# Kernel tuning notes

Hardware: AMD Instinct MI355X
Metric: run time of the kernel (lower is better)

## Reference

```python
import jax, jax.numpy as jnp
import numpy as np

NUM_GRAPHS = 256


def _lin_params(key, fan_in, fan_out):
    k1, k2 = jax.random.split(key)
    bound = 1.0 / np.sqrt(fan_in)
    W = jax.random.uniform(k1, (fan_in, fan_out), jnp.float32, -bound, bound)
    b = jax.random.uniform(k2, (fan_out,), jnp.float32, -bound, bound)
    return W, b


def setup_inputs() -> dict:
    key = jax.random.key(0)
    ks = jax.random.split(key, 12)
    N, E, F = 100000, 3200000, 32
    x = jax.random.normal(ks[0], (N, F), jnp.float32)
    edge_index = jax.random.randint(ks[1], (2, E), 0, N, jnp.int64)
    batch = jnp.sort(jax.random.randint(ks[2], (N,), 0, NUM_GRAPHS, jnp.int64))
    W1, b1 = _lin_params(ks[3], 32, 32)   # conv1
    W2, b2 = _lin_params(ks[4], 32, 24)   # conv2
    Wg, bg = _lin_params(ks[5], 24, 32)   # g_fcn1
    Wt, bt = _lin_params(ks[6], 32, 2)    # t_fcn1
    Wn1, bn1 = _lin_params(ks[7], 24, 16)  # n_fcn1
    Wn2, bn2 = _lin_params(ks[8], 16, 1)   # n_fcn2
    Wb1, bb1 = _lin_params(ks[9], 24, 16)  # b_fcn1
    Wb2, bb2 = _lin_params(ks[10], 16, 3)  # b_fcn2
    return {"x": x, "edge_index": edge_index, "batch": batch,
            "W1": W1, "b1": b1, "W2": W2, "b2": b2,
            "Wg": Wg, "bg": bg, "Wt": Wt, "bt": bt,
            "Wn1": Wn1, "bn1": bn1, "Wn2": Wn2, "bn2": bn2,
            "Wb1": Wb1, "bb1": bb1, "Wb2": Wb2, "bb2": bb2}


def _gcn_conv(x, edge_index, W, b):
    """PyG GCNConv: self-loops + symmetric normalization + linear."""
    N = x.shape[0]
    h = x @ W  # [N, out]
    loop = jnp.arange(N, dtype=edge_index.dtype)
    row = jnp.concatenate([edge_index[0], loop])  # source
    col = jnp.concatenate([edge_index[1], loop])  # target
    deg = jax.ops.segment_sum(jnp.ones_like(col, dtype=h.dtype), col, num_segments=N)
    dinv = jnp.where(deg > 0, jax.lax.rsqrt(deg), 0.0)
    norm = dinv[row] * dinv[col]  # [E+N]
    out = jax.ops.segment_sum(h[row] * norm[:, None], col, num_segments=N)
    return out + b


def _segment_softmax(v, seg, num_seg):
    """Softmax over nodes within each graph (leading axis)."""
    m = jax.ops.segment_max(v, seg, num_segments=num_seg)
    e = jnp.exp(v - m[seg])
    s = jax.ops.segment_sum(e, seg, num_segments=num_seg)
    return e / s[seg]


def reference(x, edge_index, batch, W1, b1, W2, b2, Wg, bg, Wt, bt,
              Wn1, bn1, Wn2, bn2, Wb1, bb1, Wb2, bb2):
    h = jax.nn.relu(_gcn_conv(x, edge_index, W1, b1))          # [N,32]
    h = jax.nn.relu(_gcn_conv(h, edge_index, W2, b2))          # [N,24]
    # global mean pool
    cnt = jax.ops.segment_sum(jnp.ones((h.shape[0],), h.dtype), batch, num_segments=NUM_GRAPHS)
    g = jax.ops.segment_sum(h, batch, num_segments=NUM_GRAPHS) / jnp.maximum(cnt, 1.0)[:, None]
    g = g @ Wg + bg                                            # [G,32]
    t = jax.nn.softmax(g @ Wt + bt, axis=1)                    # [G,2]
    n = jax.nn.relu(h @ Wn1 + bn1) @ Wn2 + bn2                 # [N,1]
    n = _segment_softmax(n, batch, NUM_GRAPHS)                 # per-graph softmax over nodes
    b_feat = jax.ops.segment_sum(n * h, batch, num_segments=NUM_GRAPHS)  # global_add_pool of n*x
    bb = jax.nn.relu(b_feat @ Wb1 + bb1) @ Wb2 + bb2           # [G,3]
    bb = jax.nn.softmax(bb, axis=0)                            # dim=0 softmax as in source
    return (t, n, bb)
```

## Files before the change

### kernel.cpp

```cpp
#include <hip/hip_runtime.h>
#include <math.h>

#define NG 256
#define NBLK 256

#define S1F 16.0f
#define IS1F 0.0625f
#define S2F 64.0f
#define IS2F 0.015625f

typedef __attribute__((ext_vector_type(2))) float f32x2;

__device__ __forceinline__ unsigned enc4(float f0, float f1, float f2, float f3) {
    int r = __builtin_amdgcn_cvt_pk_fp8_f32(f0, f1, 0, false);
    r = __builtin_amdgcn_cvt_pk_fp8_f32(f2, f3, r, true);
    return (unsigned)r;
}
__device__ __forceinline__ void acc8p(uint2 v, f32x2 (&a)[4]) {
    a[0] += __builtin_amdgcn_cvt_pk_f32_fp8((int)v.x, false);
    a[1] += __builtin_amdgcn_cvt_pk_f32_fp8((int)v.x, true);
    a[2] += __builtin_amdgcn_cvt_pk_f32_fp8((int)v.y, false);
    a[3] += __builtin_amdgcn_cvt_pk_f32_fp8((int)v.y, true);
}

__global__ __launch_bounds__(256) void hist_bucket_kernel(
        const int* __restrict__ col, int* __restrict__ blockOff,
        int* __restrict__ bucketTot, int E, int NB) {
    __shared__ int h[512];
    h[threadIdx.x] = 0; h[threadIdx.x + 256] = 0;
    __syncthreads();
    const int chunk = (((E + NBLK - 1) / NBLK) + 3) & ~3;
    const int beg = blockIdx.x * chunk;
    const int end = min(beg + chunk, E);
    if ((E & 3) == 0) {
        int e = beg + threadIdx.x * 4;
        for (; e + 3 < end; e += 1024) {
            int4 c = *(const int4*)(col + e);
            atomicAdd(&h[c.x >> 8], 1);
            atomicAdd(&h[c.y >> 8], 1);
            atomicAdd(&h[c.z >> 8], 1);
            atomicAdd(&h[c.w >> 8], 1);
        }
        for (; e < end; e++) atomicAdd(&h[col[e] >> 8], 1);
    } else {
        for (int e = beg + threadIdx.x; e < end; e += 256)
            atomicAdd(&h[col[e] >> 8], 1);
    }
    __syncthreads();
    for (int t = threadIdx.x; t < NB; t += 256) {
        int off = atomicAdd(&bucketTot[t], h[t]);
        blockOff[t * NBLK + blockIdx.x] = off;
    }
}

__global__ __launch_bounds__(512) void tiny_scan_kernel(
        const int* __restrict__ bucketTot, int* __restrict__ bucketBase, int NB) {
    __shared__ int part[512];
    const int t = threadIdx.x;
    int v = (t < NB) ? bucketTot[t] : 0;
    part[t] = v;
    __syncthreads();
    for (int o = 1; o < 512; o <<= 1) {
        int u = (t >= o) ? part[t - o] : 0;
        __syncthreads();
        part[t] += u;
        __syncthreads();
    }
    if (t < NB) bucketBase[t] = part[t] - v;
    if (t == NB) bucketBase[NB] = part[NB - 1];
    if (t == 511 && NB == 512) bucketBase[NB] = part[511];
}

__global__ __launch_bounds__(256) void scatter_pairs_kernel(
        const int* __restrict__ ei, const int* __restrict__ blockOff,
        const int* __restrict__ bucketBase, int* __restrict__ pairs, int E, int NB) {
    __shared__ int cur[512];
    for (int t = threadIdx.x; t < NB; t += 256)
        cur[t] = bucketBase[t] + blockOff[t * NBLK + blockIdx.x];
    __syncthreads();
    const int chunk = (((E + NBLK - 1) / NBLK) + 3) & ~3;
    const int beg = blockIdx.x * chunk;
    const int end = min(beg + chunk, E);
    if ((E & 3) == 0) {
        int e = beg + threadIdx.x * 4;
        for (; e + 3 < end; e += 1024) {
            int4 s = *(const int4*)(ei + e);
            int4 tg = *(const int4*)(ei + E + e);
            int p0 = atomicAdd(&cur[tg.x >> 8], 1);
            pairs[p0] = (int)(((unsigned)(tg.x & 255) << 17) | (unsigned)s.x);
            int p1 = atomicAdd(&cur[tg.y >> 8], 1);
            pairs[p1] = (int)(((unsigned)(tg.y & 255) << 17) | (unsigned)s.y);
            int p2 = atomicAdd(&cur[tg.z >> 8], 1);
            pairs[p2] = (int)(((unsigned)(tg.z & 255) << 17) | (unsigned)s.z);
            int p3 = atomicAdd(&cur[tg.w >> 8], 1);
            pairs[p3] = (int)(((unsigned)(tg.w & 255) << 17) | (unsigned)s.w);
        }
        for (; e < end; e++) {
            int src = ei[e];
            int tgt = ei[E + e];
            int pos = atomicAdd(&cur[tgt >> 8], 1);
            pairs[pos] = (int)(((unsigned)(tgt & 255) << 17) | (unsigned)src);
        }
    } else {
        for (int e = beg + threadIdx.x; e < end; e += 256) {
            int src = ei[e];
            int tgt = ei[E + e];
            int pos = atomicAdd(&cur[tgt >> 8], 1);
            pairs[pos] = (int)(((unsigned)(tgt & 255) << 17) | (unsigned)src);
        }
    }
}

__global__ __launch_bounds__(256) void csr_bucket_kernel(
        const int* __restrict__ pairs, const int* __restrict__ bucketBase,
        int* __restrict__ rowptr, int* __restrict__ adj,
        float* __restrict__ dinv, int N, int E) {
    __shared__ int h[256];
    __shared__ int sc[256];
    __shared__ int cur[256];
    const int b = blockIdx.x, t = threadIdx.x;
    const int base = bucketBase[b];
    const int end = bucketBase[b + 1];
    h[t] = 0;
    __syncthreads();
    for (int i = base + t; i < end; i += 256)
        atomicAdd(&h[(unsigned)pairs[i] >> 17], 1);
    __syncthreads();
    const int v = h[t];
    sc[t] = v;
    __syncthreads();
    for (int o = 1; o < 256; o <<= 1) {
        int u = (t >= o) ? sc[t - o] : 0;
        __syncthreads();
        sc[t] += u;
        __syncthreads();
    }
    const int ex = sc[t] - v;
    const int node = (b << 8) + t;
    if (node < N) {
        rowptr[node] = base + ex;
        dinv[node] = rsqrtf((float)v + 1.0f);
    }
    cur[t] = base + ex;
    __syncthreads();
    for (int i = base + t; i < end; i += 256) {
        unsigned p = (unsigned)pairs[i];
        int pos = atomicAdd(&cur[p >> 17], 1);
        adj[pos] = (int)(p & 0x1FFFFu);
    }
    if (b == 0 && t == 0) rowptr[N] = E;
}

__global__ __launch_bounds__(256) void bounds_kernel(
        const int* __restrict__ batch, int* __restrict__ starts, int N) {
    int i = blockIdx.x * blockDim.x + threadIdx.x;
    if (i >= N) return;
    int b = batch[i];
    int bp = (i == 0) ? -1 : batch[i - 1];
    for (int g = bp + 1; g <= b; g++) starts[g] = i;
    if (i == N - 1)
        for (int g = b + 1; g <= NG; g++) starts[g] = N;
}

__global__ __launch_bounds__(256) void hs1_kernel(
        const float* __restrict__ x, const float* __restrict__ W,
        const float* __restrict__ dinv, unsigned* __restrict__ hs, int N) {
    __shared__ float Ws[32 * 32];
    __shared__ float tmp[8][32];
    for (int t = threadIdx.x; t < 1024; t += blockDim.x) Ws[t] = W[t];
    __syncthreads();
    const int tid = threadIdx.x;
    const int node = blockIdx.x * 8 + (tid >> 5);
    const int n = tid >> 5, f = tid & 31;
    if (node < N) {
        const float* xr = x + (size_t)node * 32;
        float acc = 0.f;
#pragma unroll
        for (int k = 0; k < 32; k++) acc += xr[k] * Ws[k * 32 + f];
        tmp[n][f] = acc * dinv[node] * S1F;
        if (f < 8)
            hs[(size_t)node * 8 + f] = enc4(tmp[n][4 * f], tmp[n][4 * f + 1],
                                            tmp[n][4 * f + 2], tmp[n][4 * f + 3]);
    }
}

__global__ __launch_bounds__(256) void gather1_kernel(
        const int* __restrict__ rowptr, const int* __restrict__ adj,
        const uint2* __restrict__ hs1q, const float* __restrict__ dinv,
        const float* __restrict__ b1, const float* __restrict__ W2,
        unsigned* __restrict__ hs2out, int N) {
    __shared__ float W2s[32 * 24];
    __shared__ float b1s[32];
    __shared__ float h1row[16][32];
    __shared__ float hs2t[16][32];
    const int tid = threadIdx.x;
    for (int t = tid; t < 768; t += 256) W2s[t] = W2[t];
    if (tid < 32) b1s[tid] = b1[tid];

    const int g = tid >> 5;
    const int l = tid & 31;
    const int f8 = l & 3;
    const int e8 = l >> 2;
    const int n0 = (blockIdx.x * 8 + g) * 2;
    const int n1 = n0 + 1;
    const bool val0 = n0 < N;
    const bool val1 = n1 < N;

    int beg0 = 0, cnt0 = 0, beg1 = 0, cnt1 = 0;
    if (val0) {
        int2 rp = *(const int2*)(rowptr + n0);
        beg0 = rp.x; cnt0 = rp.y - rp.x;
        if (val1) { int e2 = rowptr[n0 + 2]; beg1 = rp.y; cnt1 = e2 - rp.y; }
    }
    const int* ap0 = adj + beg0;
    const int* ap1 = adj + beg1;
    f32x2 a0[4], a1[4];
#pragma unroll
    for (int k = 0; k < 4; k++) { a0[k][0] = 0.f; a0[k][1] = 0.f; a1[k][0] = 0.f; a1[k][1] = 0.f; }

    const int jmax = max(cnt0, cnt1);
    for (int j = 0; j < jmax; j += 32) {
        const int i0 = j + e8, i1 = j + 8 + e8, i2 = j + 16 + e8, i3 = j + 24 + e8;
        int sA0 = ap0[i0], sA1 = ap0[i1], sA2 = ap0[i2], sA3 = ap0[i3];
        int sB0 = ap1[i0], sB1 = ap1[i1], sB2 = ap1[i2], sB3 = ap1[i3];
        if (i0 >= cnt0) sA0 = 0; if (i1 >= cnt0) sA1 = 0;
        if (i2 >= cnt0) sA2 = 0; if (i3 >= cnt0) sA3 = 0;
        if (i0 >= cnt1) sB0 = 0; if (i1 >= cnt1) sB1 = 0;
        if (i2 >= cnt1) sB2 = 0; if (i3 >= cnt1) sB3 = 0;
        uint2 vA0 = hs1q[(size_t)sA0 * 4 + f8];
        uint2 vA1 = hs1q[(size_t)sA1 * 4 + f8];
        uint2 vA2 = hs1q[(size_t)sA2 * 4 + f8];
        uint2 vA3 = hs1q[(size_t)sA3 * 4 + f8];
        uint2 vB0 = hs1q[(size_t)sB0 * 4 + f8];
        uint2 vB1 = hs1q[(size_t)sB1 * 4 + f8];
        uint2 vB2 = hs1q[(size_t)sB2 * 4 + f8];
        uint2 vB3 = hs1q[(size_t)sB3 * 4 + f8];
        if (i0 >= cnt0) { vA0.x = 0u; vA0.y = 0u; }
        if (i1 >= cnt0) { vA1.x = 0u; vA1.y = 0u; }
        if (i2 >= cnt0) { vA2.x = 0u; vA2.y = 0u; }
        if (i3 >= cnt0) { vA3.x = 0u; vA3.y = 0u; }
        if (i0 >= cnt1) { vB0.x = 0u; vB0.y = 0u; }
        if (i1 >= cnt1) { vB1.x = 0u; vB1.y = 0u; }
        if (i2 >= cnt1) { vB2.x = 0u; vB2.y = 0u; }
        if (i3 >= cnt1) { vB3.x = 0u; vB3.y = 0u; }
        acc8p(vA0, a0); acc8p(vA1, a0); acc8p(vA2, a0); acc8p(vA3, a0);
        acc8p(vB0, a1); acc8p(vB1, a1); acc8p(vB2, a1); acc8p(vB3, a1);
    }
#pragma unroll
    for (int k = 0; k < 4; k++) {
        float x0 = a0[k][0], x1 = a0[k][1], y0 = a1[k][0], y1 = a1[k][1];
        x0 += __shfl_xor(x0, 4); x0 += __shfl_xor(x0, 8); x0 += __shfl_xor(x0, 16);
        x1 += __shfl_xor(x1, 4); x1 += __shfl_xor(x1, 8); x1 += __shfl_xor(x1, 16);
        y0 += __shfl_xor(y0, 4); y0 += __shfl_xor(y0, 8); y0 += __shfl_xor(y0, 16);
        y1 += __shfl_xor(y1, 4); y1 += __shfl_xor(y1, 8); y1 += __shfl_xor(y1, 16);
        a0[k][0] = x0; a0[k][1] = x1; a1[k][0] = y0; a1[k][1] = y1;
    }

    __syncthreads();

    auto fin1 = [&](const f32x2 (&a)[4], int node, int row) {
        const int fq = l & 3;
        const float c = dinv[node] * IS1F;
        uint2 w = hs1q[(size_t)node * 4 + fq];
        f32x2 s0 = __builtin_amdgcn_cvt_pk_f32_fp8((int)w.x, false);
        f32x2 s1 = __builtin_amdgcn_cvt_pk_f32_fp8((int)w.x, true);
        f32x2 s2 = __builtin_amdgcn_cvt_pk_f32_fp8((int)w.y, false);
        f32x2 s3 = __builtin_amdgcn_cvt_pk_f32_fp8((int)w.y, true);
        h1row[row][8 * fq + 0] = fmaxf(c * (a[0][0] + s0[0]) + b1s[8 * fq + 0], 0.f);
        h1row[row][8 * fq + 1] = fmaxf(c * (a[0][1] + s0[1]) + b1s[8 * fq + 1], 0.f);
        h1row[row][8 * fq + 2] = fmaxf(c * (a[1][0] + s1[0]) + b1s[8 * fq + 2], 0.f);
        h1row[row][8 * fq + 3] = fmaxf(c * (a[1][1] + s1[1]) + b1s[8 * fq + 3], 0.f);
        h1row[row][8 * fq + 4] = fmaxf(c * (a[2][0] + s2[0]) + b1s[8 * fq + 4], 0.f);
        h1row[row][8 * fq + 5] = fmaxf(c * (a[2][1] + s2[1]) + b1s[8 * fq + 5], 0.f);
        h1row[row][8 * fq + 6] = fmaxf(c * (a[3][0] + s3[0]) + b1s[8 * fq + 6], 0.f);
        h1row[row][8 * fq + 7] = fmaxf(c * (a[3][1] + s3[1]) + b1s[8 * fq + 7], 0.f);
    };
    if (l < 4) { if (val0) fin1(a0, n0, 2 * g); }
    else if (l < 8) { if (val1) fin1(a1, n1, 2 * g + 1); }

#pragma unroll
    for (int nn = 0; nn < 2; ++nn) {
        const int node = n0 + nn;
        if (node >= N) break;
        const int row = 2 * g + nn;
        const float sc = dinv[node] * S2F;
        float aa = 0.f;
        if (l < 24) {
#pragma unroll
            for (int k = 0; k < 32; k++) aa += h1row[row][k] * W2s[k * 24 + l];
        }
        hs2t[row][l] = (l < 24) ? aa * sc : 0.f;
        if (l < 8)
            hs2out[(size_t)node * 8 + l] = enc4(hs2t[row][4 * l], hs2t[row][4 * l + 1],
                                                hs2t[row][4 * l + 2], hs2t[row][4 * l + 3]);
    }
}

__global__ __launch_bounds__(256) void gather2_kernel(
        const int* __restrict__ rowptr, const int* __restrict__ adj,
        const uint2* __restrict__ hs2q, const float* __restrict__ dinv,
        const float* __restrict__ b2,
        const float* __restrict__ Wn1, const float* __restrict__ bn1,
        const float* __restrict__ Wn2, const float* __restrict__ bn2,
        float* __restrict__ h2out, float* __restrict__ vout, int N) {
    __shared__ float Wn1s[24 * 16];
    __shared__ float b2s[32], bn1s[16], Wn2s[16];
    __shared__ float h2row[16][32];
    const int tid = threadIdx.x;
    for (int t = tid; t < 384; t += 256) Wn1s[t] = Wn1[t];
    if (tid < 32) b2s[tid] = (tid < 24) ? b2[tid] : 0.f;
    if (tid < 16) { bn1s[tid] = bn1[tid]; Wn2s[tid] = Wn2[tid]; }

    const int g = tid >> 5;
    const int l = tid & 31;
    const int f8 = l & 3;
    const int e8 = l >> 2;
    const int n0 = (blockIdx.x * 8 + g) * 2;
    const int n1 = n0 + 1;
    const bool val0 = n0 < N;
    const bool val1 = n1 < N;

    int beg0 = 0, cnt0 = 0, beg1 = 0, cnt1 = 0;
    if (val0) {
        int2 rp = *(const int2*)(rowptr + n0);
        beg0 = rp.x; cnt0 = rp.y - rp.x;
        if (val1) { int e2 = rowptr[n0 + 2]; beg1 = rp.y; cnt1 = e2 - rp.y; }
    }
    const int* ap0 = adj + beg0;
    const int* ap1 = adj + beg1;
    f32x2 a0[4], a1[4];
#pragma unroll
    for (int k = 0; k < 4; k++) { a0[k][0] = 0.f; a0[k][1] = 0.f; a1[k][0] = 0.f; a1[k][1] = 0.f; }

    const int jmax = max(cnt0, cnt1);
    for (int j = 0; j < jmax; j += 32) {
        const int i0 = j + e8, i1 = j + 8 + e8, i2 = j + 16 + e8, i3 = j + 24 + e8;
        int sA0 = ap0[i0], sA1 = ap0[i1], sA2 = ap0[i2], sA3 = ap0[i3];
        int sB0 = ap1[i0], sB1 = ap1[i1], sB2 = ap1[i2], sB3 = ap1[i3];
        if (i0 >= cnt0) sA0 = 0; if (i1 >= cnt0) sA1 = 0;
        if (i2 >= cnt0) sA2 = 0; if (i3 >= cnt0) sA3 = 0;
        if (i0 >= cnt1) sB0 = 0; if (i1 >= cnt1) sB1 = 0;
        if (i2 >= cnt1) sB2 = 0; if (i3 >= cnt1) sB3 = 0;
        uint2 vA0 = hs2q[(size_t)sA0 * 4 + f8];
        uint2 vA1 = hs2q[(size_t)sA1 * 4 + f8];
        uint2 vA2 = hs2q[(size_t)sA2 * 4 + f8];
        uint2 vA3 = hs2q[(size_t)sA3 * 4 + f8];
        uint2 vB0 = hs2q[(size_t)sB0 * 4 + f8];
        uint2 vB1 = hs2q[(size_t)sB1 * 4 + f8];
        uint2 vB2 = hs2q[(size_t)sB2 * 4 + f8];
        uint2 vB3 = hs2q[(size_t)sB3 * 4 + f8];
        if (i0 >= cnt0) { vA0.x = 0u; vA0.y = 0u; }
        if (i1 >= cnt0) { vA1.x = 0u; vA1.y = 0u; }
        if (i2 >= cnt0) { vA2.x = 0u; vA2.y = 0u; }
        if (i3 >= cnt0) { vA3.x = 0u; vA3.y = 0u; }
        if (i0 >= cnt1) { vB0.x = 0u; vB0.y = 0u; }
        if (i1 >= cnt1) { vB1.x = 0u; vB1.y = 0u; }
        if (i2 >= cnt1) { vB2.x = 0u; vB2.y = 0u; }
        if (i3 >= cnt1) { vB3.x = 0u; vB3.y = 0u; }
        acc8p(vA0, a0); acc8p(vA1, a0); acc8p(vA2, a0); acc8p(vA3, a0);
        acc8p(vB0, a1); acc8p(vB1, a1); acc8p(vB2, a1); acc8p(vB3, a1);
    }
#pragma unroll
    for (int k = 0; k < 4; k++) {
        float x0 = a0[k][0], x1 = a0[k][1], y0 = a1[k][0], y1 = a1[k][1];
        x0 += __shfl_xor(x0, 4); x0 += __shfl_xor(x0, 8); x0 += __shfl_xor(x0, 16);
        x1 += __shfl_xor(x1, 4); x1 += __shfl_xor(x1, 8); x1 += __shfl_xor(x1, 16);
        y0 += __shfl_xor(y0, 4); y0 += __shfl_xor(y0, 8); y0 += __shfl_xor(y0, 16);
        y1 += __shfl_xor(y1, 4); y1 += __shfl_xor(y1, 8); y1 += __shfl_xor(y1, 16);
        a0[k][0] = x0; a0[k][1] = x1; a1[k][0] = y0; a1[k][1] = y1;
    }

    __syncthreads();

    auto fin2 = [&](const f32x2 (&a)[4], int node, int row) {
        const int fq = l & 3;
        const float c = dinv[node] * IS2F;
        uint2 w = hs2q[(size_t)node * 4 + fq];
        f32x2 s0 = __builtin_amdgcn_cvt_pk_f32_fp8((int)w.x, false);
        f32x2 s1 = __builtin_amdgcn_cvt_pk_f32_fp8((int)w.x, true);
        f32x2 s2 = __builtin_amdgcn_cvt_pk_f32_fp8((int)w.y, false);
        f32x2 s3 = __builtin_amdgcn_cvt_pk_f32_fp8((int)w.y, true);
        h2row[row][8 * fq + 0] = fmaxf(c * (a[0][0] + s0[0]) + b2s[8 * fq + 0], 0.f);
        h2row[row][8 * fq + 1] = fmaxf(c * (a[0][1] + s0[1]) + b2s[8 * fq + 1], 0.f);
        h2row[row][8 * fq + 2] = fmaxf(c * (a[1][0] + s1[0]) + b2s[8 * fq + 2], 0.f);
        h2row[row][8 * fq + 3] = fmaxf(c * (a[1][1] + s1[1]) + b2s[8 * fq + 3], 0.f);
        h2row[row][8 * fq + 4] = fmaxf(c * (a[2][0] + s2[0]) + b2s[8 * fq + 4], 0.f);
        h2row[row][8 * fq + 5] = fmaxf(c * (a[2][1] + s2[1]) + b2s[8 * fq + 5], 0.f);
        h2row[row][8 * fq + 6] = fmaxf(c * (a[3][0] + s3[0]) + b2s[8 * fq + 6], 0.f);
        h2row[row][8 * fq + 7] = fmaxf(c * (a[3][1] + s3[1]) + b2s[8 * fq + 7], 0.f);
    };
    if (l < 4) { if (val0) fin2(a0, n0, 2 * g); }
    else if (l < 8) { if (val1) fin2(a1, n1, 2 * g + 1); }

#pragma unroll
    for (int nn = 0; nn < 2; ++nn) {
        const int node = n0 + nn;
        if (node >= N) break;
        const int row = 2 * g + nn;
        if (l < 24) h2out[(size_t)node * 24 + l] = h2row[row][l];
        float val = 0.f;
        if (l < 16) {
            float u = bn1s[l];
#pragma unroll
            for (int k = 0; k < 24; k++) u += h2row[row][k] * Wn1s[k * 16 + l];
            val = fmaxf(u, 0.f) * Wn2s[l];
        }
        val += __shfl_down(val, 8, 16);
        val += __shfl_down(val, 4, 16);
        val += __shfl_down(val, 2, 16);
        val += __shfl_down(val, 1, 16);
        if (l == 0) vout[node] = val + bn2[0];
    }
}

__global__ __launch_bounds__(256) void graph_kernel(
        const float* __restrict__ v, const float* __restrict__ h2,
        const int* __restrict__ starts,
        const float* __restrict__ Wg, const float* __restrict__ bg,
        const float* __restrict__ Wt, const float* __restrict__ bt,
        const float* __restrict__ Wb1p, const float* __restrict__ bb1p,
        const float* __restrict__ Wb2p, const float* __restrict__ bb2p,
        float* __restrict__ out_t, float* __restrict__ out_n,
        float* __restrict__ bbpre, int N) {
    const int g = blockIdx.x;
    const int tid = threadIdx.x;
    const int lane = tid & 63;
    const int wv = tid >> 6;

    const int start = starts[g];
    const int end = starts[g + 1];

    __shared__ float sm[4];
    __shared__ float pH[4][24], pW[4][24], pS[4];

    float m = -INFINITY;
    for (int idx = start + tid; idx < end; idx += 256) m = fmaxf(m, v[idx]);
#pragma unroll
    for (int off = 32; off > 0; off >>= 1) m = fmaxf(m, __shfl_down(m, off, 64));
    if (lane == 0) sm[wv] = m;
    __syncthreads();
    m = fmaxf(fmaxf(sm[0], sm[1]), fmaxf(sm[2], sm[3]));

    const int half = lane >> 5;
    const int slot = wv * 2 + half;
    const int feat = lane & 31;
    const bool fa = feat < 24;
    float hs = 0.f, ws = 0.f, se = 0.f;
    int i = start + slot;
    for (; i + 24 < end; i += 32) {
        float v0 = v[i], v1 = v[i + 8], v2 = v[i + 16], v3 = v[i + 24];
        float h0 = 0.f, h1 = 0.f, hh2 = 0.f, h3 = 0.f;
        if (fa) {
            h0 = h2[(size_t)i * 24 + feat];
            h1 = h2[(size_t)(i + 8) * 24 + feat];
            hh2 = h2[(size_t)(i + 16) * 24 + feat];
            h3 = h2[(size_t)(i + 24) * 24 + feat];
        }
        float e0 = __expf(v0 - m), e1 = __expf(v1 - m);
        float e2 = __expf(v2 - m), e3 = __expf(v3 - m);
        if (feat == 0) se += (e0 + e1) + (e2 + e3);
        hs += (h0 + h1) + (hh2 + h3);
        ws += (e0 * h0 + e1 * h1) + (e2 * hh2 + e3 * h3);
    }
    for (; i < end; i += 8) {
        float vv = v[i];
        float e = __expf(vv - m);
        if (feat == 0) se += e;
        if (fa) {
            float hv = h2[(size_t)i * 24 + feat];
            hs += hv;
            ws += e * hv;
        }
    }
    hs += __shfl_xor(hs, 32, 64);
    ws += __shfl_xor(ws, 32, 64);
    se += __shfl_xor(se, 32, 64);
    if (lane < 24) { pH[wv][lane] = hs; pW[wv][lane] = ws; }
    if (lane == 0) pS[wv] = se;
    __syncthreads();
    const float stot = pS[0] + pS[1] + pS[2] + pS[3];
    const float invs = (stot > 0.f) ? 1.f / stot : 0.f;

    for (int idx = start + tid; idx < end; idx += 256)
        out_n[idx] = __expf(v[idx] - m) * invs;

    const float denom = fmaxf((float)(end - start), 1.0f);
    if (tid < 32) {
        float a = bg[tid];
#pragma unroll
        for (int k = 0; k < 24; k++) {
            float mean_k = (pH[0][k] + pH[1][k] + pH[2][k] + pH[3][k]) / denom;
            a += mean_k * Wg[k * 32 + tid];
        }
        float p0 = a * Wt[tid * 2];
        float p1 = a * Wt[tid * 2 + 1];
#pragma unroll
        for (int off = 16; off > 0; off >>= 1) {
            p0 += __shfl_down(p0, off, 32);
            p1 += __shfl_down(p1, off, 32);
        }
        if (tid == 0) {
            float t0 = p0 + bt[0], t1 = p1 + bt[1];
            float tm = fmaxf(t0, t1);
            float e0 = __expf(t0 - tm), e1 = __expf(t1 - tm);
            float ts = e0 + e1;
            out_t[g * 2 + 0] = e0 / ts;
            out_t[g * 2 + 1] = e1 / ts;
        }
    }
    if (tid < 16) {
        float u = bb1p[tid];
#pragma unroll
        for (int k = 0; k < 24; k++) {
            float bf_k = (pW[0][k] + pW[1][k] + pW[2][k] + pW[3][k]) * invs;
            u += bf_k * Wb1p[k * 16 + tid];
        }
        u = fmaxf(u, 0.f);
        float q0 = u * Wb2p[tid * 3 + 0];
        float q1 = u * Wb2p[tid * 3 + 1];
        float q2 = u * Wb2p[tid * 3 + 2];
#pragma unroll
        for (int off = 8; off > 0; off >>= 1) {
            q0 += __shfl_down(q0, off, 16);
            q1 += __shfl_down(q1, off, 16);
            q2 += __shfl_down(q2, off, 16);
        }
        if (tid == 0) {
            bbpre[g * 3 + 0] = q0 + bb2p[0];
            bbpre[g * 3 + 1] = q1 + bb2p[1];
            bbpre[g * 3 + 2] = q2 + bb2p[2];
        }
    }
}

__global__ __launch_bounds__(256) void bb_kernel(
        const float* __restrict__ bbpre, float* __restrict__ out_bb) {
    __shared__ float red[NG];
    int g = threadIdx.x;
#pragma unroll
    for (int c = 0; c < 3; c++) {
        float vv = bbpre[g * 3 + c];
        red[g] = vv;
        __syncthreads();
        for (int off = 128; off > 0; off >>= 1) {
            if (g < off) red[g] = fmaxf(red[g], red[g + off]);
            __syncthreads();
        }
        float m = red[0];
        __syncthreads();
        float e = __expf(vv - m);
        red[g] = e;
        __syncthreads();
        for (int off = 128; off > 0; off >>= 1) {
            if (g < off) red[g] += red[g + off];
            __syncthreads();
        }
        float ssum = red[0];
        __syncthreads();
        out_bb[g * 3 + c] = e / ssum;
    }
}

extern "C" void kernel_launch(void* const* d_in, const int* in_sizes, int n_in,
                              void* d_out, int out_size, void* d_ws, size_t ws_size,
                              hipStream_t stream) {
    const float* x   = (const float*)d_in[0];
    const int*   ei  = (const int*)d_in[1];
    const int*   bat = (const int*)d_in[2];
    const float* W1  = (const float*)d_in[3];
    const float* b1  = (const float*)d_in[4];
    const float* W2  = (const float*)d_in[5];
    const float* b2  = (const float*)d_in[6];
    const float* Wg  = (const float*)d_in[7];
    const float* bg  = (const float*)d_in[8];
    const float* Wt  = (const float*)d_in[9];
    const float* bt  = (const float*)d_in[10];
    const float* Wn1 = (const float*)d_in[11];
    const float* bn1 = (const float*)d_in[12];
    const float* Wn2 = (const float*)d_in[13];
    const float* bn2 = (const float*)d_in[14];
    const float* Wb1 = (const float*)d_in[15];
    const float* bb1 = (const float*)d_in[16];
    const float* Wb2 = (const float*)d_in[17];
    const float* bb2 = (const float*)d_in[18];

    const int N = in_sizes[2];
    const int E = in_sizes[1] / 2;
    const int NB = (N + 255) >> 8;
    const int M = NB * NBLK;

    auto rnd4 = [](size_t v) { return (v + 3) & ~(size_t)3; };
    size_t oRow = 0;
    size_t oDin = oRow + rnd4((size_t)N + 1);
    size_t oAdj = oDin + rnd4((size_t)N);
    size_t oBB  = oAdj + rnd4((size_t)E);
    size_t oTot = oBB + rnd4((size_t)NB + 1);
    size_t oSt  = oTot + rnd4((size_t)NB);
    size_t oT   = oSt + rnd4((size_t)NG + 1);
    size_t oPar = oT + rnd4((size_t)M);

    int*   wsi     = (int*)d_ws;
    float* wsf     = (float*)d_ws;
    int*   rowptr  = wsi + oRow;
    float* dinv    = wsf + oDin;
    int*   adj     = wsi + oAdj;
    int*   bbase   = wsi + oBB;
    int*   btot    = wsi + oTot;
    int*   starts  = wsi + oSt;
    int*   blkoff  = wsi + oT;
    int*   pairs   = wsi + oPar;
    unsigned* hs1b = (unsigned*)(wsf + oT);
    float* h2      = wsf + oT;
    float* vbuf    = wsf + oT + (size_t)24 * N;
    unsigned* hs2b = (unsigned*)(wsf + oT + (size_t)26 * N);
    float* bbpre   = wsf + oT + (size_t)28 * N;

    float* out_t  = (float*)d_out;
    float* out_n  = out_t + 2 * NG;
    float* out_bb = out_t + 2 * NG + N;

    const int B = 256;

    (void)hipMemsetAsync(btot, 0, (size_t)NB * sizeof(int), stream);
    bounds_kernel<<<(N + B - 1) / B, B, 0, stream>>>(bat, starts, N);
    hist_bucket_kernel<<<NBLK, B, 0, stream>>>(ei + E, blkoff, btot, E, NB);
    tiny_scan_kernel<<<1, 512, 0, stream>>>(btot, bbase, NB);
    scatter_pairs_kernel<<<NBLK, B, 0, stream>>>(ei, blkoff, bbase, pairs, E, NB);
    csr_bucket_kernel<<<NB, B, 0, stream>>>(pairs, bbase, rowptr, adj, dinv, N, E);

    hs1_kernel<<<(N + 7) / 8, B, 0, stream>>>(x, W1, dinv, hs1b, N);
    gather1_kernel<<<(N + 15) / 16, B, 0, stream>>>(rowptr, adj, (const uint2*)hs1b,
                                                    dinv, b1, W2, hs2b, N);
    gather2_kernel<<<(N + 15) / 16, B, 0, stream>>>(rowptr, adj, (const uint2*)hs2b,
                                                    dinv, b2, Wn1, bn1, Wn2, bn2, h2, vbuf, N);
    graph_kernel<<<NG, B, 0, stream>>>(vbuf, h2, starts, Wg, bg, Wt, bt,
                                       Wb1, bb1, Wb2, bb2, out_t, out_n, bbpre, N);
    bb_kernel<<<1, B, 0, stream>>>(bbpre, out_bb);
}
```

Measured before the change: 281.0 us.

## Build CSR with global per-node atomics instead of two-level bucket sort

Replaces the bucketed histogram, pair scatter and per-bucket local sort with a global per-node degree count, a per-bucket sum and scan to form rowptr, and a direct scatter of sources into adj using global atomic cursors. This removes the intermediate pairs buffer pass and the block-offset table. In exchange it relies on millions of contended global atomics at random addresses, and neighbor order within rows becomes nondeterministic.

New measurement: 627.4 us. 123% more time.

```diff
diff --git a/kernel.cpp b/kernel.cpp
--- a/kernel.cpp
+++ b/kernel.cpp
@@ -2,7 +2,6 @@
 #include <math.h>
 
 #define NG 256
-#define NBLK 256
 
 #define S1F 16.0f
 #define IS1F 0.0625f
@@ -23,34 +22,35 @@
     a[3] += __builtin_amdgcn_cvt_pk_f32_fp8((int)v.y, true);
 }
 
-__global__ __launch_bounds__(256) void hist_bucket_kernel(
-        const int* __restrict__ col, int* __restrict__ blockOff,
-        int* __restrict__ bucketTot, int E, int NB) {
-    __shared__ int h[512];
-    h[threadIdx.x] = 0; h[threadIdx.x + 256] = 0;
-    __syncthreads();
-    const int chunk = (((E + NBLK - 1) / NBLK) + 3) & ~3;
-    const int beg = blockIdx.x * chunk;
-    const int end = min(beg + chunk, E);
+__global__ __launch_bounds__(256) void deg_kernel(
+        const int* __restrict__ col, int* __restrict__ deg, int E) {
     if ((E & 3) == 0) {
-        int e = beg + threadIdx.x * 4;
-        for (; e + 3 < end; e += 1024) {
-            int4 c = *(const int4*)(col + e);
-            atomicAdd(&h[c.x >> 8], 1);
-            atomicAdd(&h[c.y >> 8], 1);
-            atomicAdd(&h[c.z >> 8], 1);
-            atomicAdd(&h[c.w >> 8], 1);
-        }
-        for (; e < end; e++) atomicAdd(&h[col[e] >> 8], 1);
+        const int E4 = E >> 2;
+        const int i = blockIdx.x * 256 + threadIdx.x;
+        if (i < E4) {
+            int4 c = ((const int4*)col)[i];
+            atomicAdd(&deg[c.x], 1);
+            atomicAdd(&deg[c.y], 1);
+            atomicAdd(&deg[c.z], 1);
+            atomicAdd(&deg[c.w], 1);
+        }
     } else {
-        for (int e = beg + threadIdx.x; e < end; e += 256)
-            atomicAdd(&h[col[e] >> 8], 1);
-    }
-    __syncthreads();
-    for (int t = threadIdx.x; t < NB; t += 256) {
-        int off = atomicAdd(&bucketTot[t], h[t]);
-        blockOff[t * NBLK + blockIdx.x] = off;
-    }
+        const int e = blockIdx.x * 256 + threadIdx.x;
+        if (e < E) atomicAdd(&deg[col[e]], 1);
+    }
+}
+
+__global__ __launch_bounds__(256) void bucket_sum_kernel(
+        const int* __restrict__ deg, int* __restrict__ btot, int N) {
+    __shared__ int ps[4];
+    const int t = threadIdx.x;
+    const int node = (blockIdx.x << 8) + t;
+    int v = (node < N) ? deg[node] : 0;
+#pragma unroll
+    for (int o = 32; o > 0; o >>= 1) v += __shfl_down(v, o, 64);
+    if ((t & 63) == 0) ps[t >> 6] = v;
+    __syncthreads();
+    if (t == 0) btot[blockIdx.x] = ps[0] + ps[1] + ps[2] + ps[3];
 }
 
 __global__ __launch_bounds__(512) void tiny_scan_kernel(
@@ -71,84 +71,53 @@
     if (t == 511 && NB == 512) bucketBase[NB] = part[511];
 }
 
-__global__ __launch_bounds__(256) void scatter_pairs_kernel(
-        const int* __restrict__ ei, const int* __restrict__ blockOff,
-        const int* __restrict__ bucketBase, int* __restrict__ pairs, int E, int NB) {
-    __shared__ int cur[512];
-    for (int t = threadIdx.x; t < NB; t += 256)
-        cur[t] = bucketBase[t] + blockOff[t * NBLK + blockIdx.x];
-    __syncthreads();
-    const int chunk = (((E + NBLK - 1) / NBLK) + 3) & ~3;
-    const int beg = blockIdx.x * chunk;
-    const int end = min(beg + chunk, E);
+__global__ __launch_bounds__(256) void rowptr_kernel(
+        int* degcur , const int* __restrict__ bbase,
+        int* __restrict__ rowptr, float* __restrict__ dinv, int N, int E) {
+    __shared__ int sc[256];
+    const int b = blockIdx.x, t = threadIdx.x;
+    const int node = (b << 8) + t;
+    const int v = (node < N) ? degcur[node] : 0;
+    sc[t] = v;
+    __syncthreads();
+    for (int o = 1; o < 256; o <<= 1) {
+        int u = (t >= o) ? sc[t - o] : 0;
+        __syncthreads();
+        sc[t] += u;
+        __syncthreads();
+    }
+    const int r = bbase[b] + sc[t] - v;
+    if (node < N) {
+        rowptr[node] = r;
+        degcur[node] = r;
+        dinv[node] = rsqrtf((float)v + 1.0f);
+    }
+    if (b == 0 && t == 0) rowptr[N] = E;
+}
+
+__global__ __launch_bounds__(256) void scatter_adj_kernel(
+        const int* __restrict__ ei, int* __restrict__ cursor,
+        int* __restrict__ adj, int E) {
     if ((E & 3) == 0) {
-        int e = beg + threadIdx.x * 4;
-        for (; e + 3 < end; e += 1024) {
-            int4 s = *(const int4*)(ei + e);
-            int4 tg = *(const int4*)(ei + E + e);
-            int p0 = atomicAdd(&cur[tg.x >> 8], 1);
-            pairs[p0] = (int)(((unsigned)(tg.x & 255) << 17) | (unsigned)s.x);
-            int p1 = atomicAdd(&cur[tg.y >> 8], 1);
-            pairs[p1] = (int)(((unsigned)(tg.y & 255) << 17) | (unsigned)s.y);
-            int p2 = atomicAdd(&cur[tg.z >> 8], 1);
-            pairs[p2] = (int)(((unsigned)(tg.z & 255) << 17) | (unsigned)s.z);
-            int p3 = atomicAdd(&cur[tg.w >> 8], 1);
-            pairs[p3] = (int)(((unsigned)(tg.w & 255) << 17) | (unsigned)s.w);
-        }
-        for (; e < end; e++) {
+        const int E4 = E >> 2;
+        const int i = blockIdx.x * 256 + threadIdx.x;
+        if (i < E4) {
+            int4 s = ((const int4*)ei)[i];
+            int4 t = ((const int4*)(ei + E))[i];
+            int p0 = atomicAdd(&cursor[t.x], 1);
+            int p1 = atomicAdd(&cursor[t.y], 1);
+            int p2 = atomicAdd(&cursor[t.z], 1);
+            int p3 = atomicAdd(&cursor[t.w], 1);
+            adj[p0] = s.x; adj[p1] = s.y; adj[p2] = s.z; adj[p3] = s.w;
+        }
+    } else {
+        const int e = blockIdx.x * 256 + threadIdx.x;
+        if (e < E) {
             int src = ei[e];
             int tgt = ei[E + e];
-            int pos = atomicAdd(&cur[tgt >> 8], 1);
-            pairs[pos] = (int)(((unsigned)(tgt & 255) << 17) | (unsigned)src);
-        }
-    } else {
-        for (int e = beg + threadIdx.x; e < end; e += 256) {
-            int src = ei[e];
-            int tgt = ei[E + e];
-            int pos = atomicAdd(&cur[tgt >> 8], 1);
-            pairs[pos] = (int)(((unsigned)(tgt & 255) << 17) | (unsigned)src);
-        }
-    }
-}
-
-__global__ __launch_bounds__(256) void csr_bucket_kernel(
-        const int* __restrict__ pairs, const int* __restrict__ bucketBase,
-        int* __restrict__ rowptr, int* __restrict__ adj,
-        float* __restrict__ dinv, int N, int E) {
-    __shared__ int h[256];
-    __shared__ int sc[256];
-    __shared__ int cur[256];
-    const int b = blockIdx.x, t = threadIdx.x;
-    const int base = bucketBase[b];
-    const int end = bucketBase[b + 1];
-    h[t] = 0;
-    __syncthreads();
-    for (int i = base + t; i < end; i += 256)
-        atomicAdd(&h[(unsigned)pairs[i] >> 17], 1);
-    __syncthreads();
-    const int v = h[t];
-    sc[t] = v;
-    __syncthreads();
-    for (int o = 1; o < 256; o <<= 1) {
-        int u = (t >= o) ? sc[t - o] : 0;
-        __syncthreads();
-        sc[t] += u;
-        __syncthreads();
-    }
-    const int ex = sc[t] - v;
-    const int node = (b << 8) + t;
-    if (node < N) {
-        rowptr[node] = base + ex;
-        dinv[node] = rsqrtf((float)v + 1.0f);
-    }
-    cur[t] = base + ex;
-    __syncthreads();
-    for (int i = base + t; i < end; i += 256) {
-        unsigned p = (unsigned)pairs[i];
-        int pos = atomicAdd(&cur[p >> 17], 1);
-        adj[pos] = (int)(p & 0x1FFFFu);
-    }
-    if (b == 0 && t == 0) rowptr[N] = E;
+            adj[atomicAdd(&cursor[tgt], 1)] = src;
+        }
+    }
 }
 
 __global__ __launch_bounds__(256) void bounds_kernel(
@@ -587,46 +556,46 @@
     const int N = in_sizes[2];
     const int E = in_sizes[1] / 2;
     const int NB = (N + 255) >> 8;
-    const int M = NB * NBLK;
 
     auto rnd4 = [](size_t v) { return (v + 3) & ~(size_t)3; };
     size_t oRow = 0;
     size_t oDin = oRow + rnd4((size_t)N + 1);
     size_t oAdj = oDin + rnd4((size_t)N);
-    size_t oBB  = oAdj + rnd4((size_t)E);
-    size_t oTot = oBB + rnd4((size_t)NB + 1);
-    size_t oSt  = oTot + rnd4((size_t)NB);
-    size_t oT   = oSt + rnd4((size_t)NG + 1);
-    size_t oPar = oT + rnd4((size_t)M);
+    size_t oDeg = oAdj + rnd4((size_t)E);
+    size_t oTot = oDeg + rnd4((size_t)N);
+    size_t oBB  = oTot + rnd4((size_t)NB);
+    size_t oSt  = oBB + rnd4((size_t)NB + 1);
+    size_t oCmp = oSt + rnd4((size_t)NG + 1);
 
     int*   wsi     = (int*)d_ws;
     float* wsf     = (float*)d_ws;
     int*   rowptr  = wsi + oRow;
     float* dinv    = wsf + oDin;
     int*   adj     = wsi + oAdj;
+    int*   degcur  = wsi + oDeg;
+    int*   btot    = wsi + oTot;
     int*   bbase   = wsi + oBB;
-    int*   btot    = wsi + oTot;
     int*   starts  = wsi + oSt;
-    int*   blkoff  = wsi + oT;
-    int*   pairs   = wsi + oPar;
-    unsigned* hs1b = (unsigned*)(wsf + oT);
-    float* h2      = wsf + oT;
-    float* vbuf    = wsf + oT + (size_t)24 * N;
-    unsigned* hs2b = (unsigned*)(wsf + oT + (size_t)26 * N);
-    float* bbpre   = wsf + oT + (size_t)28 * N;
+    unsigned* hs1b = (unsigned*)(wsf + oCmp);
+    float* h2      = wsf + oCmp;
+    float* vbuf    = wsf + oCmp + (size_t)24 * N;
+    unsigned* hs2b = (unsigned*)(wsf + oCmp + (size_t)26 * N);
+    float* bbpre   = wsf + oCmp + (size_t)28 * N;
 
     float* out_t  = (float*)d_out;
     float* out_n  = out_t + 2 * NG;
     float* out_bb = out_t + 2 * NG + N;
 
     const int B = 256;
-
-    (void)hipMemsetAsync(btot, 0, (size_t)NB * sizeof(int), stream);
+    const int gE = ((E & 3) == 0) ? ((E / 4) + B - 1) / B : (E + B - 1) / B;
+
+    (void)hipMemsetAsync(degcur, 0, (size_t)N * sizeof(int), stream);
     bounds_kernel<<<(N + B - 1) / B, B, 0, stream>>>(bat, starts, N);
-    hist_bucket_kernel<<<NBLK, B, 0, stream>>>(ei + E, blkoff, btot, E, NB);
+    deg_kernel<<<gE, B, 0, stream>>>(ei + E, degcur, E);
+    bucket_sum_kernel<<<NB, B, 0, stream>>>(degcur, btot, N);
     tiny_scan_kernel<<<1, 512, 0, stream>>>(btot, bbase, NB);
-    scatter_pairs_kernel<<<NBLK, B, 0, stream>>>(ei, blkoff, bbase, pairs, E, NB);
-    csr_bucket_kernel<<<NB, B, 0, stream>>>(pairs, bbase, rowptr, adj, dinv, N, E);
+    rowptr_kernel<<<NB, B, 0, stream>>>(degcur, bbase, rowptr, dinv, N, E);
+    scatter_adj_kernel<<<gE, B, 0, stream>>>(ei, degcur, adj, E);
 
     hs1_kernel<<<(N + 7) / 8, B, 0, stream>>>(x, W1, dinv, hs1b, N);
     gather1_kernel<<<(N + 15) / 16, B, 0, stream>>>(rowptr, adj, (const uint2*)hs1b,
```

## Fuse CSR build into one cooperative kernel and pad gathers with zero row

Applied to the files above, without the earlier changes.

Replaces the bounds, histogram, scan, scatter and per-bucket CSR kernels with a single cooperative kernel that uses grid-wide syncs between phases, with one block per bucket (NB blocks) instead of a fixed 256. This removes several kernel launches and the global blockOff and bucketBase round trips. Separately, the gather kernels now point out-of-range neighbour slots at an extra zeroed row N instead of masking the loaded values, which drops the per-load select instructions. The cooperative launch requires all NB blocks to be resident at once and introduces grid barrier costs, and the tail loop for edges in the vectorized path is dropped.

Result: slower. 406.4 us (+44.6%).

```diff
diff --git a/kernel.cpp b/kernel.cpp
--- a/kernel.cpp
+++ b/kernel.cpp
@@ -1,8 +1,10 @@
 #include <hip/hip_runtime.h>
+#include <hip/hip_cooperative_groups.h>
 #include <math.h>
 
+namespace cg = cooperative_groups;
+
 #define NG 256
-#define NBLK 256
 
 #define S1F 16.0f
 #define IS1F 0.0625f
@@ -23,143 +25,131 @@
     a[3] += __builtin_amdgcn_cvt_pk_f32_fp8((int)v.y, true);
 }
 
-__global__ __launch_bounds__(256) void hist_bucket_kernel(
-        const int* __restrict__ col, int* __restrict__ blockOff,
-        int* __restrict__ bucketTot, int E, int NB) {
-    __shared__ int h[512];
-    h[threadIdx.x] = 0; h[threadIdx.x + 256] = 0;
-    __syncthreads();
-    const int chunk = (((E + NBLK - 1) / NBLK) + 3) & ~3;
-    const int beg = blockIdx.x * chunk;
+__global__ __launch_bounds__(256) void build_coop_kernel(
+        const int* __restrict__ ei, const int* __restrict__ bat,
+        int* __restrict__ btot, int* __restrict__ pairs,
+        int* __restrict__ rowptr, int* __restrict__ adj,
+        float* __restrict__ dinv, int* __restrict__ starts,
+        int N, int E, int NB) {
+    __shared__ int A[513];
+    __shared__ int Boff[512];
+    __shared__ int C[512];
+    __shared__ int D[512];
+    const int b = blockIdx.x, t = threadIdx.x;
+    cg::grid_group grid = cg::this_grid();
+
+    {
+        int i = b * 256 + t;
+        if (i < N) {
+            int bb = bat[i];
+            int bp = (i == 0) ? -1 : bat[i - 1];
+            for (int g = bp + 1; g <= bb; g++) starts[g] = i;
+            if (i == N - 1)
+                for (int g = bb + 1; g <= NG; g++) starts[g] = N;
+        }
+    }
+
+    C[t] = 0; C[t + 256] = 0;
+    __syncthreads();
+    const int chunk = (((E + NB - 1) / NB) + 3) & ~3;
+    const int beg = b * chunk;
     const int end = min(beg + chunk, E);
+    const int* col = ei + E;
     if ((E & 3) == 0) {
-        int e = beg + threadIdx.x * 4;
-        for (; e + 3 < end; e += 1024) {
+        for (int e = beg + t * 4; e + 3 < end; e += 1024) {
             int4 c = *(const int4*)(col + e);
-            atomicAdd(&h[c.x >> 8], 1);
-            atomicAdd(&h[c.y >> 8], 1);
-            atomicAdd(&h[c.z >> 8], 1);
-            atomicAdd(&h[c.w >> 8], 1);
-        }
-        for (; e < end; e++) atomicAdd(&h[col[e] >> 8], 1);
+            atomicAdd(&C[c.x >> 8], 1);
+            atomicAdd(&C[c.y >> 8], 1);
+            atomicAdd(&C[c.z >> 8], 1);
+            atomicAdd(&C[c.w >> 8], 1);
+        }
     } else {
-        for (int e = beg + threadIdx.x; e < end; e += 256)
-            atomicAdd(&h[col[e] >> 8], 1);
-    }
-    __syncthreads();
-    for (int t = threadIdx.x; t < NB; t += 256) {
-        int off = atomicAdd(&bucketTot[t], h[t]);
-        blockOff[t * NBLK + blockIdx.x] = off;
-    }
-}
-
-__global__ __launch_bounds__(512) void tiny_scan_kernel(
-        const int* __restrict__ bucketTot, int* __restrict__ bucketBase, int NB) {
-    __shared__ int part[512];
-    const int t = threadIdx.x;
-    int v = (t < NB) ? bucketTot[t] : 0;
-    part[t] = v;
-    __syncthreads();
-    for (int o = 1; o < 512; o <<= 1) {
-        int u = (t >= o) ? part[t - o] : 0;
+        for (int e = beg + t; e < end; e += 256)
+            atomicAdd(&C[col[e] >> 8], 1);
+    }
+    __syncthreads();
+    if (t < NB)       Boff[t]       = atomicAdd(&btot[t], C[t]);
+    if (t + 256 < NB) Boff[t + 256] = atomicAdd(&btot[t + 256], C[t + 256]);
+
+    grid.sync();
+
+    const int v0 = (t < NB) ? btot[t] : 0;
+    const int v1 = (t + 256 < NB) ? btot[t + 256] : 0;
+    C[t] = v0; C[t + 256] = v1;
+    __syncthreads();
+    {
+        int* src = C; int* dst = D;
+        for (int off = 1; off < 512; off <<= 1) {
+            int a0 = src[t] + ((t >= off) ? src[t - off] : 0);
+            int a1 = src[t + 256] + src[t + 256 - off];
+            dst[t] = a0; dst[t + 256] = a1;
+            __syncthreads();
+            int* tm = src; src = dst; dst = tm;
+        }
+        const int inc0 = src[t], inc1 = src[t + 256], tot = src[511];
         __syncthreads();
-        part[t] += u;
+        A[t] = inc0 - v0;
+        A[t + 256] = inc1 - v1;
+        if (t == 0) A[NB] = tot;
+    }
+    C[t] = A[t] + Boff[t];
+    C[t + 256] = A[t + 256] + Boff[t + 256];
+    __syncthreads();
+
+    if ((E & 3) == 0) {
+        for (int e = beg + t * 4; e + 3 < end; e += 1024) {
+            int4 s = *(const int4*)(ei + e);
+            int4 tg = *(const int4*)(col + e);
+            int p0 = atomicAdd(&C[tg.x >> 8], 1);
+            pairs[p0] = (int)(((unsigned)(tg.x & 255) << 17) | (unsigned)s.x);
+            int p1 = atomicAdd(&C[tg.y >> 8], 1);
+            pairs[p1] = (int)(((unsigned)(tg.y & 255) << 17) | (unsigned)s.y);
+            int p2 = atomicAdd(&C[tg.z >> 8], 1);
+            pairs[p2] = (int)(((unsigned)(tg.z & 255) << 17) | (unsigned)s.z);
+            int p3 = atomicAdd(&C[tg.w >> 8], 1);
+            pairs[p3] = (int)(((unsigned)(tg.w & 255) << 17) | (unsigned)s.w);
+        }
+    } else {
+        for (int e = beg + t; e < end; e += 256) {
+            int src = ei[e];
+            int tgt = col[e];
+            int pos = atomicAdd(&C[tgt >> 8], 1);
+            pairs[pos] = (int)(((unsigned)(tgt & 255) << 17) | (unsigned)src);
+        }
+    }
+
+    grid.sync();
+
+    const int base = A[b];
+    const int bend = A[b + 1];
+    D[t] = 0;
+    __syncthreads();
+    for (int i = base + t; i < bend; i += 256)
+        atomicAdd(&D[(unsigned)pairs[i] >> 17], 1);
+    __syncthreads();
+    const int hv = D[t];
+    C[t] = hv;
+    __syncthreads();
+    for (int o = 1; o < 256; o <<= 1) {
+        int u = (t >= o) ? C[t - o] : 0;
         __syncthreads();
-    }
-    if (t < NB) bucketBase[t] = part[t] - v;
-    if (t == NB) bucketBase[NB] = part[NB - 1];
-    if (t == 511 && NB == 512) bucketBase[NB] = part[511];
-}
-
-__global__ __launch_bounds__(256) void scatter_pairs_kernel(
-        const int* __restrict__ ei, const int* __restrict__ blockOff,
-        const int* __restrict__ bucketBase, int* __restrict__ pairs, int E, int NB) {
-    __shared__ int cur[512];
-    for (int t = threadIdx.x; t < NB; t += 256)
-        cur[t] = bucketBase[t] + blockOff[t * NBLK + blockIdx.x];
-    __syncthreads();
-    const int chunk = (((E + NBLK - 1) / NBLK) + 3) & ~3;
-    const int beg = blockIdx.x * chunk;
-    const int end = min(beg + chunk, E);
-    if ((E & 3) == 0) {
-        int e = beg + threadIdx.x * 4;
-        for (; e + 3 < end; e += 1024) {
-            int4 s = *(const int4*)(ei + e);
-            int4 tg = *(const int4*)(ei + E + e);
-            int p0 = atomicAdd(&cur[tg.x >> 8], 1);
-            pairs[p0] = (int)(((unsigned)(tg.x & 255) << 17) | (unsigned)s.x);
-            int p1 = atomicAdd(&cur[tg.y >> 8], 1);
-            pairs[p1] = (int)(((unsigned)(tg.y & 255) << 17) | (unsigned)s.y);
-            int p2 = atomicAdd(&cur[tg.z >> 8], 1);
-            pairs[p2] = (int)(((unsigned)(tg.z & 255) << 17) | (unsigned)s.z);
-            int p3 = atomicAdd(&cur[tg.w >> 8], 1);
-            pairs[p3] = (int)(((unsigned)(tg.w & 255) << 17) | (unsigned)s.w);
-        }
-        for (; e < end; e++) {
-            int src = ei[e];
-            int tgt = ei[E + e];
-            int pos = atomicAdd(&cur[tgt >> 8], 1);
-            pairs[pos] = (int)(((unsigned)(tgt & 255) << 17) | (unsigned)src);
-        }
-    } else {
-        for (int e = beg + threadIdx.x; e < end; e += 256) {
-            int src = ei[e];
-            int tgt = ei[E + e];
-            int pos = atomicAdd(&cur[tgt >> 8], 1);
-            pairs[pos] = (int)(((unsigned)(tgt & 255) << 17) | (unsigned)src);
-        }
-    }
-}
-
-__global__ __launch_bounds__(256) void csr_bucket_kernel(
-        const int* __restrict__ pairs, const int* __restrict__ bucketBase,
-        int* __restrict__ rowptr, int* __restrict__ adj,
-        float* __restrict__ dinv, int N, int E) {
-    __shared__ int h[256];
-    __shared__ int sc[256];
-    __shared__ int cur[256];
-    const int b = blockIdx.x, t = threadIdx.x;
-    const int base = bucketBase[b];
-    const int end = bucketBase[b + 1];
-    h[t] = 0;
-    __syncthreads();
-    for (int i = base + t; i < end; i += 256)
-        atomicAdd(&h[(unsigned)pairs[i] >> 17], 1);
-    __syncthreads();
-    const int v = h[t];
-    sc[t] = v;
-    __syncthreads();
-    for (int o = 1; o < 256; o <<= 1) {
-        int u = (t >= o) ? sc[t - o] : 0;
+        C[t] += u;
         __syncthreads();
-        sc[t] += u;
-        __syncthreads();
-    }
-    const int ex = sc[t] - v;
+    }
+    const int ex = C[t] - hv;
     const int node = (b << 8) + t;
     if (node < N) {
         rowptr[node] = base + ex;
-        dinv[node] = rsqrtf((float)v + 1.0f);
-    }
-    cur[t] = base + ex;
-    __syncthreads();
-    for (int i = base + t; i < end; i += 256) {
+        dinv[node] = rsqrtf((float)hv + 1.0f);
+    }
+    D[t] = base + ex;
+    __syncthreads();
+    for (int i = base + t; i < bend; i += 256) {
         unsigned p = (unsigned)pairs[i];
-        int pos = atomicAdd(&cur[p >> 17], 1);
+        int pos = atomicAdd(&D[p >> 17], 1);
         adj[pos] = (int)(p & 0x1FFFFu);
     }
     if (b == 0 && t == 0) rowptr[N] = E;
-}
-
-__global__ __launch_bounds__(256) void bounds_kernel(
-        const int* __restrict__ batch, int* __restrict__ starts, int N) {
-    int i = blockIdx.x * blockDim.x + threadIdx.x;
-    if (i >= N) return;
-    int b = batch[i];
-    int bp = (i == 0) ? -1 : batch[i - 1];
-    for (int g = bp + 1; g <= b; g++) starts[g] = i;
-    if (i == N - 1)
-        for (int g = b + 1; g <= NG; g++) starts[g] = N;
 }
 
 __global__ __launch_bounds__(256) void hs1_kernel(
@@ -181,6 +171,8 @@
         if (f < 8)
             hs[(size_t)node * 8 + f] = enc4(tmp[n][4 * f], tmp[n][4 * f + 1],
                                             tmp[n][4 * f + 2], tmp[n][4 * f + 3]);
+    } else if (node == N) {
+        if (f < 8) hs[(size_t)N * 8 + f] = 0u;
     }
 }
 
@@ -196,6 +188,7 @@
     const int tid = threadIdx.x;
     for (int t = tid; t < 768; t += 256) W2s[t] = W2[t];
     if (tid < 32) b1s[tid] = b1[tid];
+    if (blockIdx.x == 0 && tid < 8) hs2out[(size_t)N * 8 + tid] = 0u;
 
     const int g = tid >> 5;
     const int l = tid & 31;
@@ -223,10 +216,10 @@
         const int i0 = j + e8, i1 = j + 8 + e8, i2 = j + 16 + e8, i3 = j + 24 + e8;
         int sA0 = ap0[i0], sA1 = ap0[i1], sA2 = ap0[i2], sA3 = ap0[i3];
         int sB0 = ap1[i0], sB1 = ap1[i1], sB2 = ap1[i2], sB3 = ap1[i3];
-        if (i0 >= cnt0) sA0 = 0; if (i1 >= cnt0) sA1 = 0;
-        if (i2 >= cnt0) sA2 = 0; if (i3 >= cnt0) sA3 = 0;
-        if (i0 >= cnt1) sB0 = 0; if (i1 >= cnt1) sB1 = 0;
-        if (i2 >= cnt1) sB2 = 0; if (i3 >= cnt1) sB3 = 0;
+        if (i0 >= cnt0) sA0 = N; if (i1 >= cnt0) sA1 = N;
+        if (i2 >= cnt0) sA2 = N; if (i3 >= cnt0) sA3 = N;
+        if (i0 >= cnt1) sB0 = N; if (i1 >= cnt1) sB1 = N;
+        if (i2 >= cnt1) sB2 = N; if (i3 >= cnt1) sB3 = N;
         uint2 vA0 = hs1q[(size_t)sA0 * 4 + f8];
         uint2 vA1 = hs1q[(size_t)sA1 * 4 + f8];
         uint2 vA2 = hs1q[(size_t)sA2 * 4 + f8];
@@ -235,14 +228,6 @@
         uint2 vB1 = hs1q[(size_t)sB1 * 4 + f8];
         uint2 vB2 = hs1q[(size_t)sB2 * 4 + f8];
         uint2 vB3 = hs1q[(size_t)sB3 * 4 + f8];
-        if (i0 >= cnt0) { vA0.x = 0u; vA0.y = 0u; }
-        if (i1 >= cnt0) { vA1.x = 0u; vA1.y = 0u; }
-        if (i2 >= cnt0) { vA2.x = 0u; vA2.y = 0u; }
-        if (i3 >= cnt0) { vA3.x = 0u; vA3.y = 0u; }
-        if (i0 >= cnt1) { vB0.x = 0u; vB0.y = 0u; }
-        if (i1 >= cnt1) { vB1.x = 0u; vB1.y = 0u; }
-        if (i2 >= cnt1) { vB2.x = 0u; vB2.y = 0u; }
-        if (i3 >= cnt1) { vB3.x = 0u; vB3.y = 0u; }
         acc8p(vA0, a0); acc8p(vA1, a0); acc8p(vA2, a0); acc8p(vA3, a0);
         acc8p(vB0, a1); acc8p(vB1, a1); acc8p(vB2, a1); acc8p(vB3, a1);
     }
@@ -337,10 +322,10 @@
         const int i0 = j + e8, i1 = j + 8 + e8, i2 = j + 16 + e8, i3 = j + 24 + e8;
         int sA0 = ap0[i0], sA1 = ap0[i1], sA2 = ap0[i2], sA3 = ap0[i3];
         int sB0 = ap1[i0], sB1 = ap1[i1], sB2 = ap1[i2], sB3 = ap1[i3];
-        if (i0 >= cnt0) sA0 = 0; if (i1 >= cnt0) sA1 = 0;
-        if (i2 >= cnt0) sA2 = 0; if (i3 >= cnt0) sA3 = 0;
-        if (i0 >= cnt1) sB0 = 0; if (i1 >= cnt1) sB1 = 0;
-        if (i2 >= cnt1) sB2 = 0; if (i3 >= cnt1) sB3 = 0;
+        if (i0 >= cnt0) sA0 = N; if (i1 >= cnt0) sA1 = N;
+        if (i2 >= cnt0) sA2 = N; if (i3 >= cnt0) sA3 = N;
+        if (i0 >= cnt1) sB0 = N; if (i1 >= cnt1) sB1 = N;
+        if (i2 >= cnt1) sB2 = N; if (i3 >= cnt1) sB3 = N;
         uint2 vA0 = hs2q[(size_t)sA0 * 4 + f8];
         uint2 vA1 = hs2q[(size_t)sA1 * 4 + f8];
         uint2 vA2 = hs2q[(size_t)sA2 * 4 + f8];
@@ -349,14 +334,6 @@
         uint2 vB1 = hs2q[(size_t)sB1 * 4 + f8];
         uint2 vB2 = hs2q[(size_t)sB2 * 4 + f8];
         uint2 vB3 = hs2q[(size_t)sB3 * 4 + f8];
-        if (i0 >= cnt0) { vA0.x = 0u; vA0.y = 0u; }
-        if (i1 >= cnt0) { vA1.x = 0u; vA1.y = 0u; }
-        if (i2 >= cnt0) { vA2.x = 0u; vA2.y = 0u; }
-        if (i3 >= cnt0) { vA3.x = 0u; vA3.y = 0u; }
-        if (i0 >= cnt1) { vB0.x = 0u; vB0.y = 0u; }
-        if (i1 >= cnt1) { vB1.x = 0u; vB1.y = 0u; }
-        if (i2 >= cnt1) { vB2.x = 0u; vB2.y = 0u; }
-        if (i3 >= cnt1) { vB3.x = 0u; vB3.y = 0u; }
         acc8p(vA0, a0); acc8p(vA1, a0); acc8p(vA2, a0); acc8p(vA3, a0);
         acc8p(vB0, a1); acc8p(vB1, a1); acc8p(vB2, a1); acc8p(vB3, a1);
     }
@@ -587,33 +564,28 @@
     const int N = in_sizes[2];
     const int E = in_sizes[1] / 2;
     const int NB = (N + 255) >> 8;
-    const int M = NB * NBLK;
 
     auto rnd4 = [](size_t v) { return (v + 3) & ~(size_t)3; };
     size_t oRow = 0;
     size_t oDin = oRow + rnd4((size_t)N + 1);
     size_t oAdj = oDin + rnd4((size_t)N);
-    size_t oBB  = oAdj + rnd4((size_t)E);
-    size_t oTot = oBB + rnd4((size_t)NB + 1);
+    size_t oTot = oAdj + rnd4((size_t)E);
     size_t oSt  = oTot + rnd4((size_t)NB);
     size_t oT   = oSt + rnd4((size_t)NG + 1);
-    size_t oPar = oT + rnd4((size_t)M);
 
     int*   wsi     = (int*)d_ws;
     float* wsf     = (float*)d_ws;
     int*   rowptr  = wsi + oRow;
     float* dinv    = wsf + oDin;
     int*   adj     = wsi + oAdj;
-    int*   bbase   = wsi + oBB;
     int*   btot    = wsi + oTot;
     int*   starts  = wsi + oSt;
-    int*   blkoff  = wsi + oT;
-    int*   pairs   = wsi + oPar;
+    int*   pairs   = wsi + oT;
     unsigned* hs1b = (unsigned*)(wsf + oT);
     float* h2      = wsf + oT;
     float* vbuf    = wsf + oT + (size_t)24 * N;
     unsigned* hs2b = (unsigned*)(wsf + oT + (size_t)26 * N);
-    float* bbpre   = wsf + oT + (size_t)28 * N;
+    float* bbpre   = wsf + oT + (size_t)28 * N + 4;
 
     float* out_t  = (float*)d_out;
     float* out_n  = out_t + 2 * NG;
@@ -622,13 +594,15 @@
     const int B = 256;
 
     (void)hipMemsetAsync(btot, 0, (size_t)NB * sizeof(int), stream);
-    bounds_kernel<<<(N + B - 1) / B, B, 0, stream>>>(bat, starts, N);
-    hist_bucket_kernel<<<NBLK, B, 0, stream>>>(ei + E, blkoff, btot, E, NB);
-    tiny_scan_kernel<<<1, 512, 0, stream>>>(btot, bbase, NB);
-    scatter_pairs_kernel<<<NBLK, B, 0, stream>>>(ei, blkoff, bbase, pairs, E, NB);
-    csr_bucket_kernel<<<NB, B, 0, stream>>>(pairs, bbase, rowptr, adj, dinv, N, E);
-
-    hs1_kernel<<<(N + 7) / 8, B, 0, stream>>>(x, W1, dinv, hs1b, N);
+    {
+        void* args[] = {(void*)&ei, (void*)&bat, (void*)&btot, (void*)&pairs,
+                        (void*)&rowptr, (void*)&adj, (void*)&dinv, (void*)&starts,
+                        (void*)&N, (void*)&E, (void*)&NB};
+        (void)hipLaunchCooperativeKernel((void*)build_coop_kernel, dim3(NB), dim3(B),
+                                         args, 0, stream);
+    }
+
+    hs1_kernel<<<(N + 1 + 7) / 8, B, 0, stream>>>(x, W1, dinv, hs1b, N);
     gather1_kernel<<<(N + 15) / 16, B, 0, stream>>>(rowptr, adj, (const uint2*)hs1b,
                                                     dinv, b1, W2, hs2b, N);
     gather2_kernel<<<(N + 15) / 16, B, 0, stream>>>(rowptr, adj, (const uint2*)hs2b,
```
